# Performance work log

Hardware: AMD Instinct MI355X
Metric: run time of the kernel (lower is better)

The kernel has to match this reference:

```python
import jax, jax.numpy as jnp
import numpy as np

B, L, C, R, DK = 8, 2048, 512, 64, 64
H = 2 * C  # hdnSize
NEG = -32767.0  # -2**15 + 1
EPS = 1e-5


def _p(key, shape, std=0.02):
    return (jax.random.normal(key, shape, dtype=jnp.float32) * std)


def setup_inputs() -> dict:
    key = jax.random.key(0)
    ks = jax.random.split(key, 16)
    inp = {
        "x": jax.random.normal(ks[0], (B, L, C), dtype=jnp.float32),
        "maskPAD": jax.random.randint(ks[1], (B, 1, L), 0, 2, dtype=jnp.int32),
        "preScores": jax.random.normal(ks[2], (B, R, R), dtype=jnp.float32),
        "Wp": _p(ks[3], (C, R)), "bp": jnp.zeros((R,), jnp.float32),
        "Wq": _p(ks[4], (C, DK)), "bq": jnp.zeros((DK,), jnp.float32),
        "Wk": _p(ks[5], (C, DK)), "bk": jnp.zeros((DK,), jnp.float32),
        "Wv": _p(ks[6], (C, H)), "bv": jnp.zeros((H,), jnp.float32),
        "Wu": _p(ks[7], (C, H)), "bu": jnp.zeros((H,), jnp.float32),
        "Wo": _p(ks[8], (H, C)), "bo": jnp.zeros((C,), jnp.float32),
        "gamma": jnp.ones((C,), jnp.float32),
        "beta": jnp.zeros((C,), jnp.float32),
    }
    return inp


def reference(x, maskPAD, preScores, Wp, bp, Wq, bq, Wk, bk, Wv, bv, Wu, bu, Wo, bo, gamma, beta):
    # GLU gate: [B,L,H]
    gate = jax.nn.silu(x @ Wu + bu)
    # pseudo-attention logits [B,L,r], masked on padded positions
    pScore = x @ Wp + bp
    pad = (maskPAD[:, 0] == 0)[..., None]  # [B,L,1]
    pScore = jnp.where(pad, NEG, pScore)
    pAlpha = jax.nn.softmax(pScore, axis=1)    # softmax over L (dim=-2)
    pAlpha_ = jax.nn.softmax(pScore, axis=-1)  # softmax over r
    # compress: px [B,r,C]  (== pAlpha.transpose(-1,-2) @ x)
    px = jnp.einsum('blr,blc->brc', pAlpha, x)
    q = jax.nn.silu(px @ Wq + bq)  # [B,r,dk]
    k = jax.nn.silu(px @ Wk + bk)  # [B,r,dk]
    v = jax.nn.silu(px @ Wv + bv)  # [B,r,H]
    scores = jnp.einsum('brd,bsd->brs', q, k) / np.sqrt(DK).astype(np.float32)
    scores = scores + preScores
    alpha = jax.nn.softmax(scores, axis=2)
    z = alpha @ v                                # [B,r,H]
    z = jnp.einsum('blr,brh->blh', pAlpha_, z)   # expand back to [B,L,H]
    z = gate * z
    z = z @ Wo + bo                              # [B,L,C]
    y = x + z
    mu = jnp.mean(y, axis=-1, keepdims=True)
    var = jnp.var(y, axis=-1, keepdims=True)
    out = (y - mu) * jax.lax.rsqrt(var + EPS) * gamma + beta
    return out
```

## Files before the change

### kernel.cpp

```cpp
#include <hip/hip_runtime.h>
#include <hip/hip_bf16.h>

constexpr int B_ = 8;
constexpr int L_ = 2048;
constexpr int C_ = 512;
constexpr int R_ = 64;
constexpr int DK_ = 64;
constexpr int H_ = 1024;
constexpr int M_ = B_ * L_;
constexpr int NQKV_ = 1152;
constexpr float NEG_ = -32767.0f;

__device__ __forceinline__ float toF(float x) { return x; }
__device__ __forceinline__ float toF(__hip_bfloat16 x) { return __bfloat162float(x); }
__device__ __forceinline__ float siluf(float v) { return v / (1.0f + __expf(-v)); }
__device__ __forceinline__ ushort bfbits(float f) {
    __hip_bfloat16 h = __float2bfloat16(f);
    union { __hip_bfloat16 h; ushort u; } cv; cv.h = h; return cv.u;
}
__device__ __forceinline__ float bf2f(ushort u) {
    union { uint u; float f; } cv; cv.u = (uint)u << 16; return cv.f;
}

typedef __attribute__((ext_vector_type(8))) short bf16x8;
typedef __attribute__((ext_vector_type(4))) float f32x4;

#define GLOBAL_AS __attribute__((address_space(1)))
#define LDS_AS    __attribute__((address_space(3)))
__device__ __forceinline__ void glds16(const ushort* g, ushort* l) {
    __builtin_amdgcn_global_load_lds((const GLOBAL_AS void*)g, (LDS_AS void*)l, 16, 0, 0);
}

#define VMCNT(n) asm volatile("s_waitcnt vmcnt(" #n ")" ::: "memory")
#define BARRIER() do { __builtin_amdgcn_s_barrier(); asm volatile("" ::: "memory"); } while (0)

template <int EPI>
__global__ __launch_bounds__(256) void mfma_gemm5(
    const ushort* __restrict__ A, const ushort* __restrict__ Bt,
    const float* __restrict__ bias,
    const float* __restrict__ residF, const ushort* __restrict__ residB,
    const int* __restrict__ mask,
    ushort* __restrict__ outB, float* __restrict__ outF, float* __restrict__ outF2,
    int Ndim, int Kdim, int gridN, long bBatch)
{
    __shared__ ushort As[3][128 * 32];
    __shared__ ushort Bs[3][128 * 32];

    const int i = blockIdx.x;
    const int G = gridDim.x >> 3;
    const int gi = (gridDim.x & 7) ? i : ((i & 7) * G + (i >> 3));
    const int nt = gi % gridN, mt = gi / gridN;
    const int m0 = mt * 128, n0 = nt * 128;

    const int tid = threadIdx.x;
    const int lane = tid & 63, w = tid >> 6;
    const int wm = (w & 1) * 64, wn = (w >> 1) * 64;
    const int lr = lane & 15, lq = lane >> 4;

    const int sr = lane >> 2;
    const int sc = (lane & 3) * 8;
    const int s0 = w * 2, s1 = w * 2 + 1;

    const ushort* Bp = Bt + (bBatch ? (long)(m0 / L_) * bBatch : 0);
    int br0 = n0 + s0 * 16 + sr; if (br0 >= Ndim) br0 = Ndim - 1;
    int br1 = n0 + s1 * 16 + sr; if (br1 >= Ndim) br1 = Ndim - 1;
    const ushort* a0p = A  + (size_t)(m0 + s0 * 16 + sr) * Kdim + sc;
    const ushort* a1p = A  + (size_t)(m0 + s1 * 16 + sr) * Kdim + sc;
    const ushort* b0p = Bp + (size_t)br0 * Kdim + sc;
    const ushort* b1p = Bp + (size_t)br1 * Kdim + sc;
    const int lo0 = s0 * 512 + lane * 8;
    const int lo1 = s1 * 512 + lane * 8;

    f32x4 acc[4][4];
#pragma unroll
    for (int a = 0; a < 4; ++a)
#pragma unroll
        for (int b = 0; b < 4; ++b) acc[a][b] = (f32x4){0.f, 0.f, 0.f, 0.f};

    glds16(a0p, &As[0][lo0]);
    glds16(a1p, &As[0][lo1]);
    glds16(b0p, &Bs[0][lo0]);
    glds16(b1p, &Bs[0][lo1]);
    if (32 < Kdim) {
        glds16(a0p + 32, &As[1][lo0]);
        glds16(a1p + 32, &As[1][lo1]);
        glds16(b0p + 32, &Bs[1][lo0]);
        glds16(b1p + 32, &Bs[1][lo1]);
    }

    int cur = 0;
    for (int k0 = 0; k0 < Kdim; k0 += 32) {
        if (k0 + 32 < Kdim) VMCNT(4); else VMCNT(0);
        BARRIER();
        if (k0 + 64 < Kdim) {
            const int nx = cur ? cur - 1 : 2;
            glds16(a0p + k0 + 64, &As[nx][lo0]);
            glds16(a1p + k0 + 64, &As[nx][lo1]);
            glds16(b0p + k0 + 64, &Bs[nx][lo0]);
            glds16(b1p + k0 + 64, &Bs[nx][lo1]);
        }
        bf16x8 af[4], bf[4];
#pragma unroll
        for (int a = 0; a < 4; ++a)
            af[a] = *(const bf16x8*)&As[cur][(wm + a * 16 + lr) * 32 + lq * 8];
#pragma unroll
        for (int b = 0; b < 4; ++b)
            bf[b] = *(const bf16x8*)&Bs[cur][(wn + b * 16 + lr) * 32 + lq * 8];
#pragma unroll
        for (int a = 0; a < 4; ++a)
#pragma unroll
            for (int b = 0; b < 4; ++b)
                acc[a][b] = __builtin_amdgcn_mfma_f32_16x16x32_bf16(af[a], bf[b], acc[a][b], 0, 0, 0);
        cur = (cur == 2) ? 0 : cur + 1;
    }

#pragma unroll
    for (int a = 0; a < 4; ++a) {
#pragma unroll
        for (int b = 0; b < 4; ++b) {
            const int col = n0 + wn + b * 16 + lr;
            if (col < Ndim) {
                const float bn = (EPI == 3) ? 0.f : bias[col];
#pragma unroll
                for (int r = 0; r < 4; ++r) {
                    const int row = m0 + wm + a * 16 + lq * 4 + r;
                    float v = acc[a][b][r];
                    if (EPI == 0) {
                        v = siluf(v + bn);
                        outB[(size_t)row * Ndim + col] = bfbits(v);
                    } else if (EPI == 2) {
                        v += bn + residF[(size_t)row * Ndim + col];
                        outB[(size_t)row * Ndim + col] = bfbits(v);
                    } else {
                        v *= bf2f(residB[(size_t)row * Ndim + col]);
                        outB[(size_t)row * Ndim + col] = bfbits(v);
                    }
                }
            }
        }
    }
}

__global__ __launch_bounds__(256) void pscore_gemm(
    const ushort* __restrict__ x16, const ushort* __restrict__ Wpt,
    const float* __restrict__ bp, const int* __restrict__ mask,
    ushort* __restrict__ pAR16, ushort* __restrict__ pALT,
    float* __restrict__ sums)
{
    __shared__ ushort As[3][64 * 32];
    __shared__ ushort Bs[3][64 * 32];

    const int i = blockIdx.x;
    const int G = gridDim.x >> 3;
    const int gi = (i & 7) * G + (i >> 3);
    const int m0 = gi * 64;

    const int tid = threadIdx.x;
    const int lane = tid & 63, w = tid >> 6;
    const int lr = lane & 15, lq = lane >> 4;
    const int sr = lane >> 2, sc = (lane & 3) * 8;

    const ushort* ap  = x16 + (size_t)(m0 + w * 16 + sr) * C_ + sc;
    const ushort* bwp = Wpt + (size_t)(w * 16 + sr) * C_ + sc;
    const int loa = w * 512 + lane * 8;

    f32x4 acc[4];
#pragma unroll
    for (int b = 0; b < 4; ++b) acc[b] = (f32x4){0.f, 0.f, 0.f, 0.f};

    glds16(ap, &As[0][loa]);
    glds16(bwp, &Bs[0][loa]);
    glds16(ap + 32, &As[1][loa]);
    glds16(bwp + 32, &Bs[1][loa]);

    int cur = 0;
    for (int k0 = 0; k0 < C_; k0 += 32) {
        if (k0 + 32 < C_) VMCNT(2); else VMCNT(0);
        BARRIER();
        if (k0 + 64 < C_) {
            const int nx = cur ? cur - 1 : 2;
            glds16(ap + k0 + 64, &As[nx][loa]);
            glds16(bwp + k0 + 64, &Bs[nx][loa]);
        }
        bf16x8 af, bf[4];
        af = *(const bf16x8*)&As[cur][(w * 16 + lr) * 32 + lq * 8];
#pragma unroll
        for (int b = 0; b < 4; ++b)
            bf[b] = *(const bf16x8*)&Bs[cur][(b * 16 + lr) * 32 + lq * 8];
#pragma unroll
        for (int b = 0; b < 4; ++b)
            acc[b] = __builtin_amdgcn_mfma_f32_16x16x32_bf16(af, bf[b], acc[b], 0, 0, 0);
        cur = (cur == 2) ? 0 : cur + 1;
    }

    const int bb = m0 >> 11;
    float colsum[4] = {0.f, 0.f, 0.f, 0.f};
#pragma unroll
    for (int r = 0; r < 4; ++r) {
        const int row = m0 + w * 16 + lq * 4 + r;
        const bool dead = (mask[row] == 0);
        const int ll = row & (L_ - 1);
        float v[4];
        float mx = -3.4e38f;
#pragma unroll
        for (int b = 0; b < 4; ++b) {
            const int col = b * 16 + lr;
            float t = acc[b][r] + bp[col];
            if (dead) t = NEG_;
            v[b] = t;
            mx = fmaxf(mx, t);
            const float eL = __expf(t);
            colsum[b] += eL;
            pALT[((size_t)bb * R_ + col) * L_ + ll] = bfbits(eL);
        }
#pragma unroll
        for (int o = 1; o < 16; o <<= 1) mx = fmaxf(mx, __shfl_xor(mx, o, 64));
        float e[4], s = 0.f;
#pragma unroll
        for (int b = 0; b < 4; ++b) { e[b] = __expf(v[b] - mx); s += e[b]; }
#pragma unroll
        for (int o = 1; o < 16; o <<= 1) s += __shfl_xor(s, o, 64);
        const float inv = 1.0f / s;
#pragma unroll
        for (int b = 0; b < 4; ++b)
            pAR16[(size_t)row * R_ + b * 16 + lr] = bfbits(e[b] * inv);
    }
#pragma unroll
    for (int b = 0; b < 4; ++b) {
        colsum[b] += __shfl_xor(colsum[b], 16, 64);
        colsum[b] += __shfl_xor(colsum[b], 32, 64);
    }
    if (lq == 0) {
#pragma unroll
        for (int b = 0; b < 4; ++b)
            atomicAdd(&sums[bb * R_ + b * 16 + lr], colsum[b]);
    }
}

__global__ __launch_bounds__(256) void qkv64(
    const ushort* __restrict__ px16, const ushort* __restrict__ Wqkvt,
    const float* __restrict__ bqkv, ushort* __restrict__ qkv16)
{
    __shared__ ushort As[3][64 * 32];
    __shared__ ushort Bs[3][64 * 32];

    const int nt = blockIdx.x % 18, mt = blockIdx.x / 18;
    const int m0 = mt * 64, n0 = nt * 64;

    const int tid = threadIdx.x;
    const int lane = tid & 63, w = tid >> 6;
    const int lr = lane & 15, lq = lane >> 4;
    const int sr = lane >> 2, sc = (lane & 3) * 8;

    const ushort* ap  = px16 + (size_t)(m0 + w * 16 + sr) * C_ + sc;
    const ushort* bwp = Wqkvt + (size_t)(n0 + w * 16 + sr) * C_ + sc;
    const int loa = w * 512 + lane * 8;

    f32x4 acc[4];
#pragma unroll
    for (int b = 0; b < 4; ++b) acc[b] = (f32x4){0.f, 0.f, 0.f, 0.f};

    glds16(ap, &As[0][loa]);
    glds16(bwp, &Bs[0][loa]);
    glds16(ap + 32, &As[1][loa]);
    glds16(bwp + 32, &Bs[1][loa]);

    int cur = 0;
    for (int k0 = 0; k0 < C_; k0 += 32) {
        if (k0 + 32 < C_) VMCNT(2); else VMCNT(0);
        BARRIER();
        if (k0 + 64 < C_) {
            const int nx = cur ? cur - 1 : 2;
            glds16(ap + k0 + 64, &As[nx][loa]);
            glds16(bwp + k0 + 64, &Bs[nx][loa]);
        }
        bf16x8 af, bf[4];
        af = *(const bf16x8*)&As[cur][(w * 16 + lr) * 32 + lq * 8];
#pragma unroll
        for (int b = 0; b < 4; ++b)
            bf[b] = *(const bf16x8*)&Bs[cur][(b * 16 + lr) * 32 + lq * 8];
#pragma unroll
        for (int b = 0; b < 4; ++b)
            acc[b] = __builtin_amdgcn_mfma_f32_16x16x32_bf16(af, bf[b], acc[b], 0, 0, 0);
        cur = (cur == 2) ? 0 : cur + 1;
    }

#pragma unroll
    for (int r = 0; r < 4; ++r) {
        const int row = m0 + w * 16 + lq * 4 + r;
#pragma unroll
        for (int b = 0; b < 4; ++b) {
            const int col = n0 + b * 16 + lr;
            qkv16[(size_t)row * NQKV_ + col] = bfbits(siluf(acc[b][r] + bqkv[col]));
        }
    }
}

__global__ __launch_bounds__(512) void fused_gate_z(
    const ushort* __restrict__ x16, const ushort* __restrict__ Wut,
    const float* __restrict__ bu,
    const ushort* __restrict__ pAR, const ushort* __restrict__ zsT,
    ushort* __restrict__ zg)
{
    __shared__ ushort As[2][256 * 32];
    __shared__ ushort Bs[2][128 * 32];

    const int i = blockIdx.x;
    const int G = gridDim.x >> 3;
    const int gi = (i & 7) * G + (i >> 3);
    constexpr int gridN = H_ / 128;
    const int nt = gi % gridN, mt = gi / gridN;
    const int m0 = mt * 256, n0 = nt * 128;

    const int tid = threadIdx.x;
    const int lane = tid & 63, w = tid >> 6;
    const int wm = (w & 3) * 64, wn = (w >> 2) * 64;
    const int lr = lane & 15, lq = lane >> 4;
    const int sr = lane >> 2, sc = (lane & 3) * 8;
    const int s0 = w * 2, s1 = w * 2 + 1;

    const int bidx = m0 >> 11;
    const ushort* a0p = x16 + (size_t)(m0 + s0 * 16 + sr) * C_ + sc;
    const ushort* a1p = x16 + (size_t)(m0 + s1 * 16 + sr) * C_ + sc;
    const ushort* b0p = Wut + (size_t)(n0 + w * 16 + sr) * C_ + sc;
    const ushort* zb  = zsT + (size_t)bidx * H_ * R_;
    const ushort* c0p = pAR + (size_t)(m0 + s0 * 16 + sr) * R_ + sc;
    const ushort* c1p = pAR + (size_t)(m0 + s1 * 16 + sr) * R_ + sc;
    const ushort* d0p = zb + (size_t)(n0 + w * 16 + sr) * R_ + sc;
    const int lo0 = s0 * 512 + lane * 8;
    const int lo1 = s1 * 512 + lane * 8;
    const int lob = w * 512 + lane * 8;

    auto stage = [&](int t, int bsel) {
        if (t < 2) {
            const int off = t * 32;
            glds16(c0p + off, &As[bsel][lo0]);
            glds16(c1p + off, &As[bsel][lo1]);
            glds16(d0p + off, &Bs[bsel][lob]);
        } else {
            const int off = (t - 2) * 32;
            glds16(a0p + off, &As[bsel][lo0]);
            glds16(a1p + off, &As[bsel][lo1]);
            glds16(b0p + off, &Bs[bsel][lob]);
        }
    };

    f32x4 acc[4][4];
#pragma unroll
    for (int a = 0; a < 4; ++a)
#pragma unroll
        for (int b = 0; b < 4; ++b) acc[a][b] = (f32x4){0.f, 0.f, 0.f, 0.f};

    uint pk[4][4][2];

    stage(0, 0);

    int cur = 0;
    for (int t = 0; t < 18; ++t) {
        __syncthreads();
        if (t + 1 < 18) stage(t + 1, cur ^ 1);
        bf16x8 af[4], bf[4];
#pragma unroll
        for (int a = 0; a < 4; ++a)
            af[a] = *(const bf16x8*)&As[cur][(wm + a * 16 + lr) * 32 + lq * 8];
#pragma unroll
        for (int b = 0; b < 4; ++b)
            bf[b] = *(const bf16x8*)&Bs[cur][(wn + b * 16 + lr) * 32 + lq * 8];
#pragma unroll
        for (int a = 0; a < 4; ++a)
#pragma unroll
            for (int b = 0; b < 4; ++b)
                acc[a][b] = __builtin_amdgcn_mfma_f32_16x16x32_bf16(af[a], bf[b], acc[a][b], 0, 0, 0);
        if (t == 1) {
#pragma unroll
            for (int a = 0; a < 4; ++a)
#pragma unroll
                for (int b = 0; b < 4; ++b) {
                    pk[a][b][0] = (uint)bfbits(acc[a][b][0]) | ((uint)bfbits(acc[a][b][1]) << 16);
                    pk[a][b][1] = (uint)bfbits(acc[a][b][2]) | ((uint)bfbits(acc[a][b][3]) << 16);
                    acc[a][b] = (f32x4){0.f, 0.f, 0.f, 0.f};
                }
        }
        cur ^= 1;
    }

#pragma unroll
    for (int a = 0; a < 4; ++a) {
#pragma unroll
        for (int b = 0; b < 4; ++b) {
            const int col = n0 + wn + b * 16 + lr;
            const float bn = bu[col];
#pragma unroll
            for (int r = 0; r < 4; ++r) {
                const int row = m0 + wm + a * 16 + lq * 4 + r;
                const ushort zu = (ushort)((r & 1) ? (pk[a][b][r >> 1] >> 16)
                                                   : (pk[a][b][r >> 1] & 0xffff));
                const float v = siluf(acc[a][b][r] + bn) * bf2f(zu);
                zg[(size_t)row * H_ + col] = bfbits(v);
            }
        }
    }
}

__global__ __launch_bounds__(256) void xw_prep(
    const float* __restrict__ x, ushort* __restrict__ x16, ushort* __restrict__ xT16,
    const float* __restrict__ Wu, const float* __restrict__ Wo, const float* __restrict__ Wp,
    const float* __restrict__ Wq, const float* __restrict__ bq,
    const float* __restrict__ Wk, const float* __restrict__ bk,
    const float* __restrict__ Wv, const float* __restrict__ bv,
    ushort* __restrict__ Wut, ushort* __restrict__ Wot, ushort* __restrict__ Wpt,
    ushort* __restrict__ Wqkvt, float* __restrict__ bqkv, float* __restrict__ sums)
{
    __shared__ float tile[32][33];
    const int tx = threadIdx.x & 31, ty = threadIdx.x >> 5;
    int id = blockIdx.x;

    if (id == 8192 + 1632) {
        sums[threadIdx.x] = 0.f;
        sums[threadIdx.x + 256] = 0.f;
        return;
    }

    if (id < 8192) {
        const int c0 = (id & 15) * 32, l0 = (id >> 4) * 32;
#pragma unroll
        for (int i = 0; i < 32; i += 8) {
            const float v = x[(size_t)(l0 + ty + i) * C_ + c0 + tx];
            tile[ty + i][tx] = v;
            x16[(size_t)(l0 + ty + i) * C_ + c0 + tx] = bfbits(v);
        }
        __syncthreads();
        const int bb = l0 >> 11, ll0 = l0 & (L_ - 1);
#pragma unroll
        for (int i = 0; i < 32; i += 8)
            xT16[((size_t)bb * C_ + c0 + ty + i) * L_ + ll0 + tx] = bfbits(tile[tx][ty + i]);
        return;
    }
    id -= 8192;

    const float* W; ushort* Wt; const float* bsrc = nullptr;
    int K, Nloc, n0, k0, nn0;
    if (id < 512) {
        W = Wu; Wt = Wut; K = 512; Nloc = 1024;
        n0 = (id & 31) * 32; k0 = (id >> 5) * 32; nn0 = n0;
    } else if (id < 1024) {
        id -= 512; W = Wo; Wt = Wot; K = 1024; Nloc = 512;
        n0 = (id & 15) * 32; k0 = (id >> 4) * 32; nn0 = n0;
    } else if (id < 1056) {
        id -= 1024; W = Wp; Wt = Wpt; K = 512; Nloc = 64;
        n0 = (id & 1) * 32; k0 = (id >> 1) * 32; nn0 = n0;
    } else {
        id -= 1056; K = 512; Wt = Wqkvt;
        n0 = (id % 36) * 32; k0 = (id / 36) * 32;
        if (n0 < 64)       { W = Wq; bsrc = bq; Nloc = 64;   nn0 = n0; }
        else if (n0 < 128) { W = Wk; bsrc = bk; Nloc = 64;   nn0 = n0 - 64; }
        else               { W = Wv; bsrc = bv; Nloc = 1024; nn0 = n0 - 128; }
    }
#pragma unroll
    for (int i = 0; i < 32; i += 8)
        tile[ty + i][tx] = W[(size_t)(k0 + ty + i) * Nloc + nn0 + tx];
    __syncthreads();
#pragma unroll
    for (int i = 0; i < 32; i += 8)
        Wt[(size_t)(n0 + ty + i) * K + k0 + tx] = bfbits(tile[tx][ty + i]);
    if (bsrc && k0 == 0 && threadIdx.x < 32) bqkv[n0 + threadIdx.x] = bsrc[nn0 + threadIdx.x];
}

__global__ __launch_bounds__(256) void compress_mfma(
    const ushort* __restrict__ pALT, const ushort* __restrict__ xT,
    float* __restrict__ parts)
{
    __shared__ ushort As[3][64 * 32];
    __shared__ ushort Bs[3][128 * 32];

    const int bidx = blockIdx.y;
    const int n0 = blockIdx.x * 128;
    const int ks = blockIdx.z;
    const int kbeg = ks * (L_ / 8), kend = kbeg + L_ / 8;
    const int tid = threadIdx.x;
    const int lane = tid & 63, w = tid >> 6;
    const int lr = lane & 15, lq = lane >> 4;
    const int sr = lane >> 2, sc = (lane & 3) * 8;
    const int wm = (w & 1) * 32, wn = (w >> 1) * 64;

    const ushort* Ab = pALT + (size_t)bidx * R_ * L_;
    const ushort* Bb = xT + (size_t)bidx * C_ * L_;

    const ushort* ap  = Ab + (size_t)(w * 16 + sr) * L_ + sc;
    const ushort* b0p = Bb + (size_t)(n0 + (2 * w) * 16 + sr) * L_ + sc;
    const ushort* b1p = Bb + (size_t)(n0 + (2 * w + 1) * 16 + sr) * L_ + sc;
    const int alo  = w * 512 + lane * 8;
    const int blo0 = (2 * w) * 512 + lane * 8;
    const int blo1 = (2 * w + 1) * 512 + lane * 8;

    auto stage = [&](int k0, int bsel) {
        glds16(ap + k0, &As[bsel][alo]);
        glds16(b0p + k0, &Bs[bsel][blo0]);
        glds16(b1p + k0, &Bs[bsel][blo1]);
    };

    f32x4 acc[2][4];
#pragma unroll
    for (int a = 0; a < 2; ++a)
#pragma unroll
        for (int b = 0; b < 4; ++b) acc[a][b] = (f32x4){0.f, 0.f, 0.f, 0.f};

    stage(kbeg, 0);
    stage(kbeg + 32, 1);

    int cur = 0;
    for (int k0 = kbeg; k0 < kend; k0 += 32) {
        if (k0 + 32 < kend) VMCNT(3); else VMCNT(0);
        BARRIER();
        if (k0 + 64 < kend) stage(k0 + 64, cur ? cur - 1 : 2);
        bf16x8 af[2], bf[4];
#pragma unroll
        for (int a = 0; a < 2; ++a)
            af[a] = *(const bf16x8*)&As[cur][(wm + a * 16 + lr) * 32 + lq * 8];
#pragma unroll
        for (int b = 0; b < 4; ++b)
            bf[b] = *(const bf16x8*)&Bs[cur][(wn + b * 16 + lr) * 32 + lq * 8];
#pragma unroll
        for (int a = 0; a < 2; ++a)
#pragma unroll
            for (int b = 0; b < 4; ++b)
                acc[a][b] = __builtin_amdgcn_mfma_f32_16x16x32_bf16(af[a], bf[b], acc[a][b], 0, 0, 0);
        cur = (cur == 2) ? 0 : cur + 1;
    }
#pragma unroll
    for (int a = 0; a < 2; ++a)
#pragma unroll
        for (int b = 0; b < 4; ++b)
#pragma unroll
            for (int r = 0; r < 4; ++r) {
                const int row = wm + a * 16 + lq * 4 + r;
                const int col = n0 + wn + b * 16 + lr;
                parts[(((size_t)ks * B_ + bidx) * R_ + row) * C_ + col] = acc[a][b][r];
            }
}

__global__ __launch_bounds__(256) void compress_reduce16(const float* __restrict__ parts,
                                                         const float* __restrict__ sums,
                                                         ushort* __restrict__ px16)
{
    const size_t i = ((size_t)blockIdx.x * 256 + threadIdx.x) * 4;
    constexpr size_t S = (size_t)B_ * R_ * C_;
    float4 s = *(const float4*)(parts + i);
#pragma unroll
    for (int k = 1; k < 8; ++k) {
        const float4 p = *(const float4*)(parts + i + (size_t)k * S);
        s.x += p.x; s.y += p.y; s.z += p.z; s.w += p.w;
    }
    const float inv = 1.0f / sums[i / C_];
    ushort4 o;
    o.x = bfbits(s.x * inv); o.y = bfbits(s.y * inv);
    o.z = bfbits(s.z * inv); o.w = bfbits(s.w * inv);
    *(ushort4*)(px16 + i) = o;
}

__global__ __launch_bounds__(256) void attn_fused(
    const ushort* __restrict__ qkv, const float* __restrict__ preS,
    ushort* __restrict__ zsT)
{
    const int b = blockIdx.x >> 6, r = blockIdx.x & 63;
    const int t = threadIdx.x;
    __shared__ float al[R_];
    if (t < 64) {
        const ushort* qr = qkv + (size_t)(b * R_ + r) * NQKV_;
        const ushort* ks = qkv + (size_t)(b * R_ + t) * NQKV_ + 64;
        float acc = 0.f;
#pragma unroll
        for (int d = 0; d < DK_; d += 4) {
            const ushort4 qa = *(const ushort4*)(qr + d);
            const ushort4 ka = *(const ushort4*)(ks + d);
            acc += bf2f(qa.x) * bf2f(ka.x) + bf2f(qa.y) * bf2f(ka.y)
                 + bf2f(qa.z) * bf2f(ka.z) + bf2f(qa.w) * bf2f(ka.w);
        }
        acc = acc * 0.125f + preS[((size_t)b * R_ + r) * R_ + t];
        float mx = acc;
#pragma unroll
        for (int o = 32; o > 0; o >>= 1) mx = fmaxf(mx, __shfl_xor(mx, o, 64));
        float e = __expf(acc - mx);
        float sm = e;
#pragma unroll
        for (int o = 32; o > 0; o >>= 1) sm += __shfl_xor(sm, o, 64);
        al[t] = e / sm;
    }
    __syncthreads();
    float acc[4] = {};
    for (int s = 0; s < R_; ++s) {
        const float a = al[s];
        const ushort4 vv = *(const ushort4*)(qkv + (size_t)(b * R_ + s) * NQKV_ + 128 + t * 4);
        acc[0] += a * bf2f(vv.x);
        acc[1] += a * bf2f(vv.y);
        acc[2] += a * bf2f(vv.z);
        acc[3] += a * bf2f(vv.w);
    }
#pragma unroll
    for (int j = 0; j < 4; ++j) {
        const int h = t * 4 + j;
        zsT[((size_t)b * H_ + h) * R_ + r] = bfbits(acc[j]);
    }
}

__global__ __launch_bounds__(256) void layernorm(const ushort* __restrict__ y,
                                                 const float* __restrict__ gamma,
                                                 const float* __restrict__ beta,
                                                 float* __restrict__ out)
{
    const int w = threadIdx.x >> 6, lane = threadIdx.x & 63;
    const size_t m = (size_t)blockIdx.x * 4 + w;
    const ushort* yr = y + m * C_ + lane * 8;
    const ushort4 p0 = *(const ushort4*)(yr);
    const ushort4 p1 = *(const ushort4*)(yr + 4);
    float v[8] = { bf2f(p0.x), bf2f(p0.y), bf2f(p0.z), bf2f(p0.w),
                   bf2f(p1.x), bf2f(p1.y), bf2f(p1.z), bf2f(p1.w) };
    float s = 0.f, q = 0.f;
#pragma unroll
    for (int j = 0; j < 8; ++j) { s += v[j]; q += v[j] * v[j]; }
#pragma unroll
    for (int o = 32; o > 0; o >>= 1) {
        s += __shfl_xor(s, o, 64);
        q += __shfl_xor(q, o, 64);
    }
    const float mu = s * (1.0f / C_);
    const float var = q * (1.0f / C_) - mu * mu;
    const float inv = rsqrtf(var + 1e-5f);
    const float4 g0 = *(const float4*)(gamma + lane * 8);
    const float4 g1 = *(const float4*)(gamma + lane * 8 + 4);
    const float4 b0 = *(const float4*)(beta + lane * 8);
    const float4 b1 = *(const float4*)(beta + lane * 8 + 4);
    float4 o0, o1;
    o0.x = (v[0] - mu) * inv * g0.x + b0.x;
    o0.y = (v[1] - mu) * inv * g0.y + b0.y;
    o0.z = (v[2] - mu) * inv * g0.z + b0.z;
    o0.w = (v[3] - mu) * inv * g0.w + b0.w;
    o1.x = (v[4] - mu) * inv * g1.x + b1.x;
    o1.y = (v[5] - mu) * inv * g1.y + b1.y;
    o1.z = (v[6] - mu) * inv * g1.z + b1.z;
    o1.w = (v[7] - mu) * inv * g1.w + b1.w;
    *(float4*)(out + m * C_ + lane * 8) = o0;
    *(float4*)(out + m * C_ + lane * 8 + 4) = o1;
}

template <typename AT, typename BT, typename RT, int ACT, int EPI>
__global__ __launch_bounds__(256) void gemm64(
    const AT* __restrict__ A, const BT* __restrict__ Bw,
    const float* __restrict__ bias, const int* __restrict__ mask,
    const RT* resid, float* __restrict__ outF, __hip_bfloat16* outB,
    int Ndim, int Kdim, long bBatchStride)
{
    __shared__ float As[16][68];
    __shared__ float Bs[16][64];
    const int tid = threadIdx.x;
    const int tx = tid & 15, ty = tid >> 4;
    const int n0 = blockIdx.x * 64, m0 = blockIdx.y * 64;
    const BT* Bp = Bw + (bBatchStride ? (long)(m0 / L_) * bBatchStride : 0);
    float acc[4][4] = {};
    for (int k0 = 0; k0 < Kdim; k0 += 16) {
#pragma unroll
        for (int s = 0; s < 4; ++s) {
            int idx = tid + s * 256;
            int am = idx >> 4, ak = idx & 15;
            As[ak][am] = toF(A[(size_t)(m0 + am) * Kdim + k0 + ak]);
        }
#pragma unroll
        for (int s = 0; s < 4; ++s) {
            int idx = tid + s * 256;
            int bk = idx >> 6, bn = idx & 63;
            Bs[bk][bn] = toF(Bp[(size_t)(k0 + bk) * Ndim + n0 + bn]);
        }
        __syncthreads();
#pragma unroll
        for (int kk = 0; kk < 16; ++kk) {
            float av[4], bv[4];
            *(float4*)av = *(const float4*)&As[kk][ty * 4];
            *(float4*)bv = *(const float4*)&Bs[kk][tx * 4];
#pragma unroll
            for (int i = 0; i < 4; ++i)
#pragma unroll
                for (int j = 0; j < 4; ++j) acc[i][j] += av[i] * bv[j];
        }
        __syncthreads();
    }
#pragma unroll
    for (int i = 0; i < 4; ++i) {
        int m = m0 + ty * 4 + i;
#pragma unroll
        for (int j = 0; j < 4; ++j) {
            int n = n0 + tx * 4 + j;
            float val = acc[i][j];
            if (EPI != 3) val += bias[n];
            if (ACT) val = siluf(val);
            if (EPI == 0) outB[(size_t)m * Ndim + n] = __float2bfloat16(val);
            else if (EPI == 1) { if (mask[m] == 0) val = NEG_; outF[(size_t)m * Ndim + n] = val; }
            else if (EPI == 2) { val += toF(resid[(size_t)m * Ndim + n]); outB[(size_t)m * Ndim + n] = __float2bfloat16(val); }
            else { val *= toF(resid[(size_t)m * Ndim + n]); outB[(size_t)m * Ndim + n] = __float2bfloat16(val); }
        }
    }
}

template <int OUT>
__global__ __launch_bounds__(64) void softmaxR(const float* __restrict__ pScore,
                                               float* __restrict__ outF,
                                               ushort* __restrict__ outU)
{
    const size_t m = blockIdx.x;
    const int t = threadIdx.x;
    float v = pScore[m * R_ + t];
    float mx = v;
#pragma unroll
    for (int o = 32; o > 0; o >>= 1) mx = fmaxf(mx, __shfl_xor(mx, o, 64));
    float e = __expf(v - mx);
    float s = e;
#pragma unroll
    for (int o = 32; o > 0; o >>= 1) s += __shfl_xor(s, o, 64);
    if (OUT == 0) outF[m * R_ + t] = e / s;
    else          outU[m * R_ + t] = bfbits(e / s);
}

__global__ __launch_bounds__(256) void softmaxL(const float* __restrict__ pScore,
                                                float* __restrict__ pAlpha)
{
    const int b = blockIdx.x >> 6, r = blockIdx.x & 63;
    const int t = threadIdx.x;
    const float* base = pScore + (size_t)b * L_ * R_ + r;
    float* out = pAlpha + (size_t)b * L_ * R_ + r;
    __shared__ float red[256];
    float mx = -3.4e38f;
    for (int l = t; l < L_; l += 256) mx = fmaxf(mx, base[(size_t)l * R_]);
    red[t] = mx; __syncthreads();
    for (int s = 128; s > 0; s >>= 1) { if (t < s) red[t] = fmaxf(red[t], red[t + s]); __syncthreads(); }
    mx = red[0]; __syncthreads();
    float sum = 0.f;
    for (int l = t; l < L_; l += 256) {
        float e = __expf(base[(size_t)l * R_] - mx);
        out[(size_t)l * R_] = e; sum += e;
    }
    red[t] = sum; __syncthreads();
    for (int s = 128; s > 0; s >>= 1) { if (t < s) red[t] += red[t + s]; __syncthreads(); }
    const float inv = 1.0f / red[0];
    for (int l = t; l < L_; l += 256) out[(size_t)l * R_] *= inv;
}

__global__ __launch_bounds__(256) void compress_part(
    const float* __restrict__ pAlpha, const float* __restrict__ x,
    float* __restrict__ parts)
{
    __shared__ float As[16][64];
    __shared__ float Bs[16][64];
    const int tid = threadIdx.x;
    const int tx = tid & 15, ty = tid >> 4;
    const int n0 = blockIdx.x * 64;
    const int ks = blockIdx.y;
    const int b  = blockIdx.z;
    const float* pa = pAlpha + (size_t)b * L_ * R_;
    const float* xb = x + (size_t)b * L_ * C_;
    float acc[4][4] = {};
    const int kbeg = ks * (L_ / 4), kend = kbeg + L_ / 4;
    for (int k0 = kbeg; k0 < kend; k0 += 16) {
#pragma unroll
        for (int s = 0; s < 4; ++s) {
            int idx = tid + s * 256;
            int kk = idx >> 6, m = idx & 63;
            As[kk][m] = pa[(size_t)(k0 + kk) * R_ + m];
        }
#pragma unroll
        for (int s = 0; s < 4; ++s) {
            int idx = tid + s * 256;
            int kk = idx >> 6, n = idx & 63;
            Bs[kk][n] = xb[(size_t)(k0 + kk) * C_ + n0 + n];
        }
        __syncthreads();
#pragma unroll
        for (int kk = 0; kk < 16; ++kk) {
            float av[4], bv[4];
            *(float4*)av = *(const float4*)&As[kk][ty * 4];
            *(float4*)bv = *(const float4*)&Bs[kk][tx * 4];
#pragma unroll
            for (int i = 0; i < 4; ++i)
#pragma unroll
                for (int j = 0; j < 4; ++j) acc[i][j] += av[i] * bv[j];
        }
        __syncthreads();
    }
#pragma unroll
    for (int i = 0; i < 4; ++i)
#pragma unroll
        for (int j = 0; j < 4; ++j)
            parts[((((size_t)ks * B_ + b) * R_) + ty * 4 + i) * C_ + n0 + tx * 4 + j] = acc[i][j];
}

__global__ __launch_bounds__(256) void compress_reduce(const float* __restrict__ parts,
                                                       float* __restrict__ px)
{
    const size_t i = (size_t)blockIdx.x * 256 + threadIdx.x;
    constexpr size_t S = (size_t)B_ * R_ * C_;
    px[i] = parts[i] + parts[i + S] + parts[i + 2 * S] + parts[i + 3 * S];
}

__global__ __launch_bounds__(256) void qkv_gemm(
    const float* __restrict__ px,
    const float* __restrict__ Wq, const float* __restrict__ bq,
    const float* __restrict__ Wk, const float* __restrict__ bk,
    const float* __restrict__ Wv, const float* __restrict__ bv,
    float* __restrict__ q, float* __restrict__ k, float* __restrict__ v)
{
    __shared__ float As[16][68];
    __shared__ float Bs[16][64];
    const int tid = threadIdx.x;
    const int tx = tid & 15, ty = tid >> 4;
    const int bx = blockIdx.x;
    const int m0 = blockIdx.y * 64;
    const float* W; const float* bias; float* dst; int Nloc, ncol0;
    if (bx == 0)      { W = Wq; bias = bq; dst = q; Nloc = 64;   ncol0 = 0; }
    else if (bx == 1) { W = Wk; bias = bk; dst = k; Nloc = 64;   ncol0 = 0; }
    else              { W = Wv; bias = bv; dst = v; Nloc = H_;   ncol0 = (bx - 2) * 64; }

    float acc[4][4] = {};
    for (int k0 = 0; k0 < C_; k0 += 16) {
#pragma unroll
        for (int s = 0; s < 4; ++s) {
            int idx = tid + s * 256;
            int am = idx >> 4, ak = idx & 15;
            As[ak][am] = px[(size_t)(m0 + am) * C_ + k0 + ak];
        }
#pragma unroll
        for (int s = 0; s < 4; ++s) {
            int idx = tid + s * 256;
            int kk = idx >> 6, bn = idx & 63;
            Bs[kk][bn] = W[(size_t)(k0 + kk) * Nloc + ncol0 + bn];
        }
        __syncthreads();
#pragma unroll
        for (int kk = 0; kk < 16; ++kk) {
            float av[4], bv4[4];
            *(float4*)av = *(const float4*)&As[kk][ty * 4];
            *(float4*)bv4 = *(const float4*)&Bs[kk][tx * 4];
#pragma unroll
            for (int i = 0; i < 4; ++i)
#pragma unroll
                for (int j = 0; j < 4; ++j) acc[i][j] += av[i] * bv4[j];
        }
        __syncthreads();
    }
#pragma unroll
    for (int i = 0; i < 4; ++i) {
        int m = m0 + ty * 4 + i;
#pragma unroll
        for (int j = 0; j < 4; ++j) {
            int n = ncol0 + tx * 4 + j;
            dst[(size_t)m * Nloc + n] = siluf(acc[i][j] + bias[n]);
        }
    }
}

template <int MODE>
__global__ __launch_bounds__(256) void attn_z(const float* __restrict__ alpha,
                                              const float* __restrict__ v,
                                              float* __restrict__ zsF,
                                              ushort* __restrict__ zsT)
{
    const int b = blockIdx.x >> 6, r = blockIdx.x & 63;
    const int t = threadIdx.x;
    __shared__ float al[R_];
    if (t < R_) al[t] = alpha[((size_t)b * R_ + r) * R_ + t];
    __syncthreads();
    float acc[4] = {};
    for (int s = 0; s < R_; ++s) {
        float a = al[s];
        const float* vr = v + ((size_t)b * R_ + s) * H_;
#pragma unroll
        for (int j = 0; j < 4; ++j) acc[j] += a * vr[t + j * 256];
    }
#pragma unroll
    for (int j = 0; j < 4; ++j) {
        const int h = t + j * 256;
        if (MODE == 0) zsF[((size_t)b * R_ + r) * H_ + h] = acc[j];
        else           zsT[((size_t)b * H_ + h) * R_ + r] = bfbits(acc[j]);
    }
}

__global__ __launch_bounds__(64) void attn_scores(
    const float* __restrict__ q, const float* __restrict__ k,
    const float* __restrict__ preS, float* __restrict__ alpha)
{
    const int b = blockIdx.x >> 6, r = blockIdx.x & 63;
    const int s = threadIdx.x;
    const float* qr = q + ((size_t)b * R_ + r) * DK_;
    const float* ks = k + ((size_t)b * R_ + s) * DK_;
    float acc = 0.f;
#pragma unroll
    for (int d = 0; d < DK_; ++d) acc += qr[d] * ks[d];
    acc = acc * 0.125f + preS[((size_t)b * R_ + r) * R_ + s];
    float mx = acc;
#pragma unroll
    for (int o = 32; o > 0; o >>= 1) mx = fmaxf(mx, __shfl_xor(mx, o, 64));
    float e = __expf(acc - mx);
    float sm = e;
#pragma unroll
    for (int o = 32; o > 0; o >>= 1) sm += __shfl_xor(sm, o, 64);
    alpha[((size_t)b * R_ + r) * R_ + s] = e / sm;
}

extern "C" void kernel_launch(void* const* d_in, const int* in_sizes, int n_in,
                              void* d_out, int out_size, void* d_ws, size_t ws_size,
                              hipStream_t stream)
{
    using bf16 = __hip_bfloat16;
    const float* x      = (const float*)d_in[0];
    const int*  maskPAD = (const int*)d_in[1];
    const float* preS   = (const float*)d_in[2];
    const float* Wp     = (const float*)d_in[3];
    const float* bp     = (const float*)d_in[4];
    const float* Wq     = (const float*)d_in[5];
    const float* bq     = (const float*)d_in[6];
    const float* Wk     = (const float*)d_in[7];
    const float* bk     = (const float*)d_in[8];
    const float* Wv     = (const float*)d_in[9];
    const float* bv     = (const float*)d_in[10];
    const float* Wu     = (const float*)d_in[11];
    const float* bu     = (const float*)d_in[12];
    const float* Wo     = (const float*)d_in[13];
    const float* bo     = (const float*)d_in[14];
    const float* gamma  = (const float*)d_in[15];
    const float* beta   = (const float*)d_in[16];
    float* out          = (float*)d_out;

    char* ws = (char*)d_ws;
    const bool bigWS = ws_size >= (size_t)52 * 1024 * 1024;

    if (bigWS) {
        bf16* zg = (bf16*)ws;
        float* parts = (float*)ws;
        char* pool = ws + (size_t)M_ * H_ * 2;
        ushort* pALT   = (ushort*)pool;
        ushort* pAR16  = pALT + (size_t)B_ * R_ * L_;
        ushort* px16   = pAR16 + (size_t)M_ * R_;
        ushort* qkv16  = px16 + (size_t)B_ * R_ * C_;
        ushort* zsT16  = qkv16 + (size_t)B_ * R_ * NQKV_;
        ushort* Wqkvt  = zsT16 + (size_t)B_ * H_ * R_;
        float*  bqkv   = (float*)(Wqkvt + (size_t)NQKV_ * C_);
        float*  sums   = bqkv + NQKV_;
        bf16*  y       = (bf16*)pool;
        ushort* Wut    = (ushort*)(pool + 18221568);
        ushort* Wot    = Wut + (size_t)C_ * H_;
        ushort* Wpt    = Wot + (size_t)C_ * H_;
        ushort* x16    = (ushort*)d_out;
        ushort* xT16   = x16 + (size_t)M_ * C_;

        xw_prep<<<8192 + 1632 + 1, 256, 0, stream>>>(
            x, x16, xT16, Wu, Wo, Wp, Wq, bq, Wk, bk, Wv, bv,
            Wut, Wot, Wpt, Wqkvt, bqkv, sums);
        pscore_gemm<<<M_ / 64, 256, 0, stream>>>(x16, Wpt, bp, maskPAD,
                                                 pAR16, pALT, sums);
        compress_mfma<<<dim3(C_ / 128, B_, 8), 256, 0, stream>>>(pALT, xT16, parts);
        compress_reduce16<<<(B_ * R_ * C_) / 1024, 256, 0, stream>>>(parts, sums, px16);
        qkv64<<<(B_ * R_ / 64) * (NQKV_ / 64), 256, 0, stream>>>(px16, Wqkvt, bqkv, qkv16);
        attn_fused<<<B_ * R_, 256, 0, stream>>>(qkv16, preS, zsT16);
        fused_gate_z<<<(H_ / 128) * (M_ / 256), 512, 0, stream>>>(
            x16, Wut, bu, pAR16, zsT16, (ushort*)zg);
        mfma_gemm5<2><<<(C_ / 128) * (M_ / 128), 256, 0, stream>>>(
            (ushort*)zg, Wot, bo, x, nullptr, nullptr, (ushort*)y, nullptr, nullptr,
            C_, H_, C_ / 128, 0);
        layernorm<<<M_ / 4, 256, 0, stream>>>((const ushort*)y, gamma, beta, out);
    } else {
        float* pScore = (float*)ws;
        float* pAL   = pScore + (size_t)M_ * R_;
        float* pAR   = pAL    + (size_t)M_ * R_;
        float* px    = pAR    + (size_t)M_ * R_;
        float* q     = px     + (size_t)B_ * R_ * C_;
        float* kk    = q      + (size_t)B_ * R_ * DK_;
        float* vv    = kk     + (size_t)B_ * R_ * DK_;
        float* alpha = vv     + (size_t)B_ * R_ * H_;
        float* zs    = alpha  + (size_t)B_ * R_ * R_;
        bf16* gate_b = (bf16*)(zs + (size_t)B_ * R_ * H_);
        bf16* y_b    = (bf16*)((char*)gate_b + (size_t)L_ * H_ * 2);

        gemm64<float, float, float, 0, 1><<<dim3(R_ / 64, M_ / 64), 256, 0, stream>>>(
            x, Wp, bp, maskPAD, (const float*)nullptr, pScore, nullptr, R_, C_, 0);
        softmaxL<<<B_ * R_, 256, 0, stream>>>(pScore, pAL);
        softmaxR<0><<<M_, 64, 0, stream>>>(pScore, pAR, nullptr);
        compress_part<<<dim3(C_ / 64, 4, B_), 256, 0, stream>>>(pAL, x, pScore);
        compress_reduce<<<(B_ * R_ * C_) / 256, 256, 0, stream>>>(pScore, px);
        qkv_gemm<<<dim3(2 + H_ / 64, (B_ * R_) / 64), 256, 0, stream>>>(
            px, Wq, bq, Wk, bk, Wv, bv, q, kk, vv);
        attn_scores<<<B_ * R_, 64, 0, stream>>>(q, kk, preS, alpha);
        attn_z<0><<<B_ * R_, 256, 0, stream>>>(alpha, vv, zs, nullptr);

        for (int b = 0; b < B_; ++b) {
            const float* xb = x + (size_t)b * L_ * C_;
            gemm64<float, float, float, 1, 0><<<dim3(H_ / 64, L_ / 64), 256, 0, stream>>>(
                xb, Wu, bu, nullptr, (const float*)nullptr, nullptr, gate_b, H_, C_, 0);
            gemm64<float, float, bf16, 0, 3><<<dim3(H_ / 64, L_ / 64), 256, 0, stream>>>(
                pAR + (size_t)b * L_ * R_, zs + (size_t)b * R_ * H_,
                nullptr, nullptr, gate_b, nullptr, gate_b, H_, R_, 0);
            gemm64<bf16, float, float, 0, 2><<<dim3(C_ / 64, L_ / 64), 256, 0, stream>>>(
                gate_b, Wo, bo, nullptr, xb, nullptr, y_b, C_, H_, 0);
            layernorm<<<L_ / 4, 256, 0, stream>>>((const ushort*)y_b, gamma, beta, out + (size_t)b * L_ * C_);
        }
    }
}
```

Baseline: 243.6 us.

## Fuse output projection GEMM with residual add and LayerNorm

Replaces the Wo GEMM (which wrote a bf16 y buffer) and the separate layernorm kernel with one kernel. Each block computes a full 64-row by 512-column tile so row statistics can be reduced in shared memory and normalized output written directly. This removes the y round trip and one launch. In exchange each block holds 64x512 tiles with 64 KB of B staging, which lowers occupancy, and the tile is smaller in M than before (64 rows vs 128), so Wo is reloaded more often.

New measurement: 264.1 us. 1.08x slower.

```diff
diff --git a/kernel.cpp b/kernel.cpp
--- a/kernel.cpp
+++ b/kernel.cpp
@@ -136,6 +136,120 @@
                         outB[(size_t)row * Ndim + col] = bfbits(v);
                     }
                 }
+            }
+        }
+    }
+}
+
+__global__ __launch_bounds__(512) void wo_ln(
+    const ushort* __restrict__ zg, const ushort* __restrict__ Wot,
+    const float* __restrict__ bo, const float* __restrict__ x,
+    const float* __restrict__ gamma, const float* __restrict__ beta,
+    float* __restrict__ out)
+{
+    __shared__ ushort As[2][64 * 32];
+    __shared__ ushort Bs[2][512 * 32];
+    __shared__ float rs[64], rq[64];
+
+    const int i = blockIdx.x;
+    const int G = gridDim.x >> 3;
+    const int gi = (i & 7) * G + (i >> 3);
+    const int m0 = gi * 64;
+
+    const int tid = threadIdx.x;
+    const int lane = tid & 63, w = tid >> 6;
+    const int lr = lane & 15, lq = lane >> 4;
+    const int sr = lane >> 2, sc = (lane & 3) * 8;
+    const int wn = w * 64;
+
+    const ushort* ap = zg + (size_t)(m0 + w * 16 + sr) * H_ + sc;
+    const int alo = w * 512 + lane * 8;
+    const ushort* b0p = Wot + (size_t)((w * 4 + 0) * 16 + sr) * H_ + sc;
+    const ushort* b1p = Wot + (size_t)((w * 4 + 1) * 16 + sr) * H_ + sc;
+    const ushort* b2p = Wot + (size_t)((w * 4 + 2) * 16 + sr) * H_ + sc;
+    const ushort* b3p = Wot + (size_t)((w * 4 + 3) * 16 + sr) * H_ + sc;
+    const int blo0 = (w * 4 + 0) * 512 + lane * 8;
+    const int blo1 = (w * 4 + 1) * 512 + lane * 8;
+    const int blo2 = (w * 4 + 2) * 512 + lane * 8;
+    const int blo3 = (w * 4 + 3) * 512 + lane * 8;
+
+    auto stage = [&](int k0, int bsel) {
+        if (w < 4) glds16(ap + k0, &As[bsel][alo]);
+        glds16(b0p + k0, &Bs[bsel][blo0]);
+        glds16(b1p + k0, &Bs[bsel][blo1]);
+        glds16(b2p + k0, &Bs[bsel][blo2]);
+        glds16(b3p + k0, &Bs[bsel][blo3]);
+    };
+
+    f32x4 acc[4][4];
+#pragma unroll
+    for (int a = 0; a < 4; ++a)
+#pragma unroll
+        for (int b = 0; b < 4; ++b) acc[a][b] = (f32x4){0.f, 0.f, 0.f, 0.f};
+
+    if (tid < 64) { rs[tid] = 0.f; rq[tid] = 0.f; }
+
+    stage(0, 0);
+
+    int cur = 0;
+    for (int k0 = 0; k0 < H_; k0 += 32) {
+        __syncthreads();
+        if (k0 + 32 < H_) stage(k0 + 32, cur ^ 1);
+        bf16x8 af[4], bf[4];
+#pragma unroll
+        for (int a = 0; a < 4; ++a)
+            af[a] = *(const bf16x8*)&As[cur][(a * 16 + lr) * 32 + lq * 8];
+#pragma unroll
+        for (int b = 0; b < 4; ++b)
+            bf[b] = *(const bf16x8*)&Bs[cur][(wn + b * 16 + lr) * 32 + lq * 8];
+#pragma unroll
+        for (int a = 0; a < 4; ++a)
+#pragma unroll
+            for (int b = 0; b < 4; ++b)
+                acc[a][b] = __builtin_amdgcn_mfma_f32_16x16x32_bf16(af[a], bf[b], acc[a][b], 0, 0, 0);
+        cur ^= 1;
+    }
+
+#pragma unroll
+    for (int a = 0; a < 4; ++a) {
+#pragma unroll
+        for (int r = 0; r < 4; ++r) {
+            const int row = a * 16 + lq * 4 + r;
+            const size_t grow = (size_t)(m0 + row);
+            float s = 0.f, q = 0.f;
+#pragma unroll
+            for (int b = 0; b < 4; ++b) {
+                const int col = wn + b * 16 + lr;
+                float v = acc[a][b][r] + bo[col] + x[grow * C_ + col];
+                acc[a][b][r] = v;
+                s += v; q += v * v;
+            }
+#pragma unroll
+            for (int o = 1; o < 16; o <<= 1) {
+                s += __shfl_xor(s, o, 64);
+                q += __shfl_xor(q, o, 64);
+            }
+            if (lr == 0) {
+                atomicAdd(&rs[row], s);
+                atomicAdd(&rq[row], q);
+            }
+        }
+    }
+    __syncthreads();
+
+#pragma unroll
+    for (int a = 0; a < 4; ++a) {
+#pragma unroll
+        for (int r = 0; r < 4; ++r) {
+            const int row = a * 16 + lq * 4 + r;
+            const size_t grow = (size_t)(m0 + row);
+            const float mu = rs[row] * (1.0f / C_);
+            const float var = rq[row] * (1.0f / C_) - mu * mu;
+            const float inv = rsqrtf(var + 1e-5f);
+#pragma unroll
+            for (int b = 0; b < 4; ++b) {
+                const int col = wn + b * 16 + lr;
+                out[grow * C_ + col] = (acc[a][b][r] - mu) * inv * gamma[col] + beta[col];
             }
         }
     }
@@ -942,7 +1056,6 @@
         ushort* Wqkvt  = zsT16 + (size_t)B_ * H_ * R_;
         float*  bqkv   = (float*)(Wqkvt + (size_t)NQKV_ * C_);
         float*  sums   = bqkv + NQKV_;
-        bf16*  y       = (bf16*)pool;
         ushort* Wut    = (ushort*)(pool + 18221568);
         ushort* Wot    = Wut + (size_t)C_ * H_;
         ushort* Wpt    = Wot + (size_t)C_ * H_;
@@ -960,10 +1073,8 @@
         attn_fused<<<B_ * R_, 256, 0, stream>>>(qkv16, preS, zsT16);
         fused_gate_z<<<(H_ / 128) * (M_ / 256), 512, 0, stream>>>(
             x16, Wut, bu, pAR16, zsT16, (ushort*)zg);
-        mfma_gemm5<2><<<(C_ / 128) * (M_ / 128), 256, 0, stream>>>(
-            (ushort*)zg, Wot, bo, x, nullptr, nullptr, (ushort*)y, nullptr, nullptr,
-            C_, H_, C_ / 128, 0);
-        layernorm<<<M_ / 4, 256, 0, stream>>>((const ushort*)y, gamma, beta, out);
+        wo_ln<<<M_ / 64, 512, 0, stream>>>(
+            (const ushort*)zg, Wot, bo, x, gamma, beta, out);
     } else {
         float* pScore = (float*)ws;
         float* pAL   = pScore + (size_t)M_ * R_;
```
